# Performance work log

Measured on AMD Instinct MI355X. Metric: run time of the kernel, lower is better.

The kernel has to match this reference:

```python
import jax, jax.numpy as jnp
import numpy as np

E = 8      # num_experts
K = 2      # top-k
DIM = 1024
DFF = 2048  # fused gate+up width; intermediate = DFF // 2 == DIM


def setup_inputs() -> dict:
    key = jax.random.key(0)
    ks = jax.random.split(key, 5)
    B, S = 4, 2048
    x = jax.random.normal(ks[0], (B, S, DIM), dtype=jnp.float32)
    Wg = jax.random.normal(ks[1], (E, DIM), dtype=jnp.float32) * 0.02
    bg = jax.random.normal(ks[2], (E,), dtype=jnp.float32) * 0.02
    w1 = jax.random.normal(ks[3], (E, DFF, DIM), dtype=jnp.float32) * 0.02
    w2 = jax.random.normal(ks[4], (E, DIM, DFF // 2), dtype=jnp.float32) * 0.02
    return {"x": x, "Wg": Wg, "bg": bg, "w1": w1, "w2": w2}


def _moe(x, Wg, bg, w1, w2):
    B, S, D = x.shape
    t = x.reshape(-1, D)                      # [T, D] tokens
    logits = t @ Wg.T + bg                    # [T, E]
    probs = jax.nn.softmax(logits, axis=-1)
    topw, topi = jax.lax.top_k(probs, K)      # [T, K]
    topw = topw / jnp.sum(topw, axis=-1, keepdims=True)  # renormalize=True
    # per-token combine weight for each expert (0 if not selected): [T, E]
    combine = jnp.sum(jax.nn.one_hot(topi, E, dtype=t.dtype) * topw[..., None], axis=1)

    def body(acc, packed):
        w1e, w2e, ce = packed                 # [DFF, D], [D, DFF//2], [T]
        h = t @ w1e.T                         # [T, DFF]
        gate, up = jnp.split(h, 2, axis=-1)   # silu_and_mul (SwiGLU)
        a = jax.nn.silu(gate) * up            # [T, DFF//2]
        o = a @ w2e.T                         # [T, D]
        return acc + ce[:, None] * o, None

    out, _ = jax.lax.scan(body, jnp.zeros_like(t), (w1, w2, combine.T))
    return out.reshape(B, S, D)


def reference(x, Wg, bg, w1, w2):
    return _moe(x, Wg, bg, w1, w2)
```

## Files before the change

### kernel.cpp

```cpp
#include <hip/hip_runtime.h>
#include <hip/hip_bf16.h>
#include <cstdint>

#define T_TOKENS 8192
#define DIM 1024
#define NEXP 8
#define DFFH 1024
#define ROWCAP 17408
#define NCHUNK 16
#define MAXMT 24
#define NGATEB 128
#define NCASTB 1920

typedef __attribute__((ext_vector_type(8))) short bf16x8;
typedef __attribute__((ext_vector_type(16))) float f32x16;

__device__ __forceinline__ ushort f2bf(float f) {
  uint32_t u = __float_as_uint(f);
  uint32_t r = (u + 0x7fffu + ((u >> 16) & 1u)) >> 16;
  return (ushort)r;
}
__device__ __forceinline__ float bf2f(ushort u) {
  return __uint_as_float(((uint32_t)u) << 16);
}

__device__ __forceinline__ void async16(const void* g, const void* l) {
  __builtin_amdgcn_global_load_lds(
      (const __attribute__((address_space(1))) void*)(uintptr_t)g,
      (__attribute__((address_space(3))) void*)(uintptr_t)l, 16, 0, 0);
}

__global__ __launch_bounds__(256) void gatecast_kernel(
    const float4* __restrict__ x4, const float4* __restrict__ Wg4,
    const float* __restrict__ bg, const float4* __restrict__ w1,
    const float4* __restrict__ w2, int* __restrict__ top2e,
    float2* __restrict__ top2w, ushort* __restrict__ xb,
    ushort* __restrict__ w1b, ushort* __restrict__ w2b,
    int* __restrict__ blkcnt ) {
  __shared__ float4 wgl[NEXP * 256];
  __shared__ int lcnt[NEXP];
  const int tid = threadIdx.x;

  if (blockIdx.x >= NGATEB) {
    const int NW1 = NEXP * 2048 * DIM / 4;
    const int NW2 = NEXP * DIM * DFFH / 4;
    const int total = NW1 + NW2;
    const int cb = blockIdx.x - NGATEB;
    for (int i = cb * 256 + tid; i < total; i += NCASTB * 256) {
      float4 v; ushort* dst;
      if (i < NW1) { v = w1[i]; dst = w1b + (size_t)i * 4; }
      else { int j = i - NW1; v = w2[j]; dst = w2b + (size_t)j * 4; }
      ushort4 o4;
      o4.x = f2bf(v.x); o4.y = f2bf(v.y); o4.z = f2bf(v.z); o4.w = f2bf(v.w);
      *(ushort4*)dst = o4;
    }
    return;
  }

  for (int i = tid; i < NEXP * 256; i += 256) wgl[i] = Wg4[i];
  if (tid < NEXP) lcnt[tid] = 0;
  __syncthreads();
  const int wave = tid >> 6, lane = tid & 63;
  const float bgsel = bg[lane & 7];
  const int t0 = (blockIdx.x * 4 + wave) * 16;
  for (int tt = 0; tt < 16; ++tt) {
    const int t = t0 + tt;
    const float4* xr = x4 + (size_t)t * 256;
    ushort4* xw = (ushort4*)(xb + (size_t)t * DIM);
    float acc[NEXP];
#pragma unroll
    for (int e = 0; e < NEXP; ++e) acc[e] = 0.f;
#pragma unroll
    for (int j = 0; j < 4; ++j) {
      float4 xv = xr[lane + j * 64];
      ushort4 o4;
      o4.x = f2bf(xv.x); o4.y = f2bf(xv.y); o4.z = f2bf(xv.z); o4.w = f2bf(xv.w);
      xw[lane + j * 64] = o4;
#pragma unroll
      for (int e = 0; e < NEXP; ++e) {
        float4 wv = wgl[e * 256 + lane + j * 64];
        acc[e] += xv.x * wv.x + xv.y * wv.y + xv.z * wv.z + xv.w * wv.w;
      }
    }
#pragma unroll
    for (int e = 0; e < NEXP; ++e) {
      float v = acc[e];
      v += __shfl_xor(v, 1); v += __shfl_xor(v, 2); v += __shfl_xor(v, 4);
      acc[e] = v;
    }
    float v = acc[0];
#pragma unroll
    for (int e = 1; e < NEXP; ++e) v = ((lane & 7) == e) ? acc[e] : v;
    v += __shfl_xor(v, 8); v += __shfl_xor(v, 16); v += __shfl_xor(v, 32);
    v += bgsel;
    float m1 = v;
    m1 = fmaxf(m1, __shfl_xor(m1, 1));
    m1 = fmaxf(m1, __shfl_xor(m1, 2));
    m1 = fmaxf(m1, __shfl_xor(m1, 4));
    unsigned long long mk = __ballot(v == m1);
    int bi = (int)(__ffsll(mk) - 1) & 7;
    float v2 = (((lane & 7) == bi) ? -1e30f : v);
    float m2 = v2;
    m2 = fmaxf(m2, __shfl_xor(m2, 1));
    m2 = fmaxf(m2, __shfl_xor(m2, 2));
    m2 = fmaxf(m2, __shfl_xor(m2, 4));
    mk = __ballot(v2 == m2);
    int si = (int)(__ffsll(mk) - 1) & 7;
    if (lane == 0) {
      float w0 = 1.f / (1.f + __expf(m2 - m1));
      top2e[t] = bi | (si << 8);
      top2w[t] = make_float2(w0, 1.f - w0);
      atomicAdd(&lcnt[bi], 1);
      atomicAdd(&lcnt[si], 1);
    }
  }
  __syncthreads();
  if (tid < NEXP) blkcnt[blockIdx.x * NEXP + tid] = lcnt[tid];
}

__global__ __launch_bounds__(512) void scatter_kernel(
    const int* __restrict__ top2e, const float2* __restrict__ top2w,
    const int* __restrict__ blkcnt, int* __restrict__ rows_token,
    float* __restrict__ rows_weight, int2* __restrict__ tok2row,
    int* __restrict__ cnt, int* __restrict__ off) {
  __shared__ int s_all[NGATEB * NEXP];
  __shared__ int s_tot[NEXP], s_pre[NEXP];
  __shared__ int s_base[NEXP];
  __shared__ int lcnt[NEXP];
  const int tid = threadIdx.x;
  const int b = blockIdx.x;
  s_all[tid] = blkcnt[tid];
  s_all[512 + tid] = blkcnt[512 + tid];
  if (tid < NEXP) lcnt[tid] = 0;
  __syncthreads();
  if (tid < NEXP) {
    int tot = 0, pre = 0;
    const int cutoff = b * (NGATEB / NCHUNK);
#pragma unroll 1
    for (int k = 0; k < NGATEB; ++k) {
      int v = s_all[k * NEXP + tid];
      tot += v;
      if (k < cutoff) pre += v;
    }
    s_tot[tid] = tot; s_pre[tid] = pre;
  }
  __syncthreads();
  if (tid == 0) {
    int o = 0;
#pragma unroll
    for (int e = 0; e < NEXP; ++e) {
      s_base[e] = o + s_pre[e];
      if (b == 0) { cnt[e] = s_tot[e]; off[e] = o; }
      o += (s_tot[e] + 127) & ~127;
    }
    if (b == 0) off[NEXP] = o;
  }
  __syncthreads();
  const int t = b * 512 + tid;
  int pk = top2e[t];
  float2 w = top2w[t];
  int e0 = pk & 255, e1 = (pk >> 8) & 255;
  int p0 = atomicAdd(&lcnt[e0], 1);
  int p1 = atomicAdd(&lcnt[e1], 1);
  int r0 = s_base[e0] + p0;
  int r1 = s_base[e1] + p1;
  rows_token[r0] = t; rows_weight[r0] = w.x;
  rows_token[r1] = t; rows_weight[r1] = w.y;
  tok2row[t] = make_int2(r0, r1);
}

__global__ __launch_bounds__(256) void mlpA_kernel(
    const ushort* __restrict__ xb, const ushort* __restrict__ w1b,
    const int* __restrict__ rows_token, const int* __restrict__ cnt,
    const int* __restrict__ off, ushort* __restrict__ abuf) {
  const int bid = blockIdx.x;
  const int e = bid & 7;
  const int pos = bid >> 3;
  const int mt = pos >> 4, nt = pos & 15;
  const int count = cnt[e];
  if (mt * 128 >= count) return;
  const int base = off[e];

  __shared__ ushort As[2][128 * 64];
  __shared__ ushort Bs[2][2][64 * 64];

  const int tid = threadIdx.x;
  const int wave = tid >> 6, lane = tid & 63;
  const int wm = wave >> 1, wn = wave & 1;
  const int cg = tid & 7;
  const int r7w = (tid >> 3) & 7;
  const int cgs = (cg ^ r7w) * 8;

  const ushort* gA[4];
#pragma unroll
  for (int i = 0; i < 4; ++i) {
    int row = i * 32 + (tid >> 3);
    int r = mt * 128 + row;
    int tok = (r < count) ? rows_token[base + r] : 0;
    gA[i] = xb + ((size_t)tok * DIM + cgs);
  }
  const ushort* gBg[2];
  const ushort* gBu[2];
#pragma unroll
  for (int i = 0; i < 2; ++i) {
    int row = i * 32 + (tid >> 3);
    gBg[i] = w1b + ((size_t)(e * 2048 + nt * 64 + row) * DIM + cgs);
    gBu[i] = w1b + ((size_t)(e * 2048 + 1024 + nt * 64 + row) * DIM + cgs);
  }

#define STAGE_A1(b_, k0_)                                             \
  {                                                                   \
    _Pragma("unroll")                                                 \
    for (int i = 0; i < 4; ++i)                                       \
      async16(gA[i] + (k0_), &As[b_][(i * 256 + wave * 64) * 8]);     \
    _Pragma("unroll")                                                 \
    for (int i = 0; i < 2; ++i) {                                     \
      async16(gBg[i] + (k0_), &Bs[b_][0][(i * 256 + wave * 64) * 8]); \
      async16(gBu[i] + (k0_), &Bs[b_][1][(i * 256 + wave * 64) * 8]); \
    }                                                                 \
  }

  f32x16 accg0 = {0,0,0,0,0,0,0,0,0,0,0,0,0,0,0,0};
  f32x16 accg1 = accg0, accu0 = accg0, accu1 = accg0;

  const int xr = (lane & 7) << 3;
  const int la31 = lane & 31;
  const int kbase = (lane >> 5) * 8;

#define COMPA(b_)                                                              \
  {                                                                            \
    _Pragma("unroll")                                                          \
    for (int kk = 0; kk < 4; ++kk) {                                           \
      const int ko = (kk * 16 + kbase) ^ xr;                                   \
      bf16x8 a0 = *(const bf16x8*)&As[b_][(wm * 64 + la31) * 64 + ko];         \
      bf16x8 a1 = *(const bf16x8*)&As[b_][(wm * 64 + 32 + la31) * 64 + ko];    \
      bf16x8 bg_ = *(const bf16x8*)&Bs[b_][0][(wn * 32 + la31) * 64 + ko];     \
      bf16x8 bu_ = *(const bf16x8*)&Bs[b_][1][(wn * 32 + la31) * 64 + ko];     \
      accg0 = __builtin_amdgcn_mfma_f32_32x32x16_bf16(a0, bg_, accg0, 0, 0, 0);\
      accg1 = __builtin_amdgcn_mfma_f32_32x32x16_bf16(a1, bg_, accg1, 0, 0, 0);\
      accu0 = __builtin_amdgcn_mfma_f32_32x32x16_bf16(a0, bu_, accu0, 0, 0, 0);\
      accu1 = __builtin_amdgcn_mfma_f32_32x32x16_bf16(a1, bu_, accu1, 0, 0, 0);\
    }                                                                          \
  }

  STAGE_A1(0, 0);
  __syncthreads();
#pragma unroll
  for (int it = 0; it < 8; ++it) {
    STAGE_A1(1, it * 128 + 64);
    COMPA(0);
    __syncthreads();
    if (it < 7) STAGE_A1(0, it * 128 + 128);
    COMPA(1);
    __syncthreads();
  }

  const int colg = nt * 64 + wn * 32 + la31;
  const size_t rbase = (size_t)(base + mt * 128 + wm * 64);
  const int rlo = 4 * (lane >> 5);
#pragma unroll
  for (int s = 0; s < 2; ++s) {
    const f32x16 g16 = s ? accg1 : accg0;
    const f32x16 u16 = s ? accu1 : accu0;
#pragma unroll
    for (int r = 0; r < 16; ++r) {
      int rr = (r & 3) + 8 * (r >> 2) + rlo;
      float g = g16[r], u = u16[r];
      float a = (g / (1.f + __expf(-g))) * u;
      abuf[(rbase + s * 32 + rr) * DFFH + colg] = f2bf(a);
    }
  }
#undef STAGE_A1
#undef COMPA
}

__global__ __launch_bounds__(256) void mlpB_kernel(
    const ushort* __restrict__ abuf, const ushort* __restrict__ w2b,
    const float* __restrict__ rows_weight, const int* __restrict__ cnt,
    const int* __restrict__ off, ushort* __restrict__ obuf) {
  const int bid = blockIdx.x;
  const int e = bid & 7;
  const int pos = bid >> 3;
  const int mt = pos >> 3, nt = pos & 7;
  const int count = cnt[e];
  if (mt * 128 >= count) return;
  const int base = off[e];

  __shared__ ushort As[2][128 * 64];
  __shared__ ushort Bs[2][128 * 64];

  const int tid = threadIdx.x;
  const int wave = tid >> 6, lane = tid & 63;
  const int wm = wave >> 1, wn = wave & 1;
  const int cg = tid & 7;
  const int r7w = (tid >> 3) & 7;
  const int cgs = (cg ^ r7w) * 8;

  const ushort* gA[4];
#pragma unroll
  for (int i = 0; i < 4; ++i) {
    int row = i * 32 + (tid >> 3);
    gA[i] = abuf + ((size_t)(base + mt * 128 + row) * DFFH + cgs);
  }
  const ushort* gB[4];
#pragma unroll
  for (int i = 0; i < 4; ++i) {
    int row = i * 32 + (tid >> 3);
    gB[i] = w2b + ((size_t)(e * 1024 + nt * 128 + row) * DFFH + cgs);
  }

#define STAGE_B1(b_, k0_)                                           \
  {                                                                 \
    _Pragma("unroll")                                               \
    for (int i = 0; i < 4; ++i) {                                   \
      async16(gA[i] + (k0_), &As[b_][(i * 256 + wave * 64) * 8]);   \
      async16(gB[i] + (k0_), &Bs[b_][(i * 256 + wave * 64) * 8]);   \
    }                                                               \
  }

  f32x16 acc00 = {0,0,0,0,0,0,0,0,0,0,0,0,0,0,0,0};
  f32x16 acc01 = acc00, acc10 = acc00, acc11 = acc00;

  const int xr = (lane & 7) << 3;
  const int la31 = lane & 31;
  const int kbase = (lane >> 5) * 8;

#define COMPB(b_)                                                              \
  {                                                                            \
    _Pragma("unroll")                                                          \
    for (int kk = 0; kk < 4; ++kk) {                                           \
      const int ko = (kk * 16 + kbase) ^ xr;                                   \
      bf16x8 a0 = *(const bf16x8*)&As[b_][(wm * 64 + la31) * 64 + ko];         \
      bf16x8 a1 = *(const bf16x8*)&As[b_][(wm * 64 + 32 + la31) * 64 + ko];    \
      bf16x8 b0 = *(const bf16x8*)&Bs[b_][(wn * 64 + la31) * 64 + ko];         \
      bf16x8 b1 = *(const bf16x8*)&Bs[b_][(wn * 64 + 32 + la31) * 64 + ko];    \
      acc00 = __builtin_amdgcn_mfma_f32_32x32x16_bf16(a0, b0, acc00, 0, 0, 0); \
      acc01 = __builtin_amdgcn_mfma_f32_32x32x16_bf16(a0, b1, acc01, 0, 0, 0); \
      acc10 = __builtin_amdgcn_mfma_f32_32x32x16_bf16(a1, b0, acc10, 0, 0, 0); \
      acc11 = __builtin_amdgcn_mfma_f32_32x32x16_bf16(a1, b1, acc11, 0, 0, 0); \
    }                                                                          \
  }

  STAGE_B1(0, 0);
  __syncthreads();
#pragma unroll
  for (int it = 0; it < 8; ++it) {
    STAGE_B1(1, it * 128 + 64);
    COMPB(0);
    __syncthreads();
    if (it < 7) STAGE_B1(0, it * 128 + 128);
    COMPB(1);
    __syncthreads();
  }

  const int rlo = 4 * (lane >> 5);
  const int colb = nt * 128 + wn * 64 + la31;
#pragma unroll
  for (int s = 0; s < 2; ++s) {
    const f32x16 c0 = s ? acc10 : acc00;
    const f32x16 c1 = s ? acc11 : acc01;
#pragma unroll
    for (int r = 0; r < 16; ++r) {
      int rr = (r & 3) + 8 * (r >> 2) + rlo;
      int lrow = mt * 128 + wm * 64 + s * 32 + rr;
      if (lrow < count) {
        float wgt = rows_weight[base + lrow];
        obuf[(size_t)(base + lrow) * DIM + colb] = f2bf(wgt * c0[r]);
        obuf[(size_t)(base + lrow) * DIM + colb + 32] = f2bf(wgt * c1[r]);
      }
    }
  }
#undef STAGE_B1
#undef COMPB
}

__global__ __launch_bounds__(256) void combine_kernel(
    const ushort* __restrict__ obuf, const int2* __restrict__ tok2row,
    float* __restrict__ out) {
  const int t = blockIdx.x;
  int2 rr = tok2row[t];
  const ushort4* p0 = (const ushort4*)(obuf + (size_t)rr.x * DIM);
  const ushort4* p1 = (const ushort4*)(obuf + (size_t)rr.y * DIM);
  float4* po = (float4*)(out + (size_t)t * DIM);
  const int c = threadIdx.x;
  ushort4 a = p0[c], b = p1[c];
  float4 o;
  o.x = bf2f(a.x) + bf2f(b.x);
  o.y = bf2f(a.y) + bf2f(b.y);
  o.z = bf2f(a.z) + bf2f(b.z);
  o.w = bf2f(a.w) + bf2f(b.w);
  po[c] = o;
}

extern "C" void kernel_launch(void* const* d_in, const int* in_sizes, int n_in,
                              void* d_out, int out_size, void* d_ws, size_t ws_size,
                              hipStream_t stream) {
  const float* x = (const float*)d_in[0];
  const float* Wg = (const float*)d_in[1];
  const float* bg = (const float*)d_in[2];
  const float* w1 = (const float*)d_in[3];
  const float* w2 = (const float*)d_in[4];
  float* out = (float*)d_out;

  char* ws = (char*)d_ws;
  ushort* xb = (ushort*)ws;
  ushort* w1b = xb + (size_t)T_TOKENS * DIM;
  ushort* w2b = w1b + (size_t)NEXP * 2048 * DIM;
  ushort* abuf = w2b + (size_t)NEXP * DIM * DFFH;
  char* p = (char*)(abuf + (size_t)ROWCAP * DFFH);
  int* top2e = (int*)p;            p += T_TOKENS * 4;
  float2* top2w = (float2*)p;      p += T_TOKENS * 8;
  int* rows_token = (int*)p;       p += ROWCAP * 4;
  float* rows_weight = (float*)p;  p += ROWCAP * 4;
  int2* tok2row = (int2*)p;        p += T_TOKENS * 8;
  int* cnt = (int*)p;              p += 32;
  int* off = (int*)p;              p += 64;
  int* blkcnt = (int*)p;           p += NGATEB * NEXP * 4;
  ushort* obuf = xb;

  gatecast_kernel<<<NGATEB + NCASTB, 256, 0, stream>>>(
      (const float4*)x, (const float4*)Wg, bg, (const float4*)w1,
      (const float4*)w2, top2e, top2w, xb, w1b, w2b, blkcnt);
  scatter_kernel<<<NCHUNK, 512, 0, stream>>>(top2e, top2w, blkcnt, rows_token,
                                             rows_weight, tok2row, cnt, off);
  mlpA_kernel<<<8 * MAXMT * 16, 256, 0, stream>>>(xb, w1b, rows_token, cnt, off, abuf);
  mlpB_kernel<<<8 * MAXMT * 8, 256, 0, stream>>>(abuf, w2b, rows_weight, cnt, off, obuf);
  combine_kernel<<<T_TOKENS, 256, 0, stream>>>(obuf, tok2row, out);
}
```

Measured before the change: 231.6 us.

## Enlarge mlpA tile to 256x128 with 512-thread blocks

The first expert GEMM (gate/up plus SwiGLU) now uses 256-row by 128-column tiles per block with 8 waves, each wave computing a 128x32 slice for both gate and up. This raises arithmetic intensity per LDS load and halves the grid, cutting redundant global and LDS traffic for the weight and token tiles. Stores are masked to the padded per-expert row count because tiles can now overrun the 128-aligned padding. The cost is more LDS per block (about 128 KB) and more accumulator registers, which lowers occupancy and increases tail waste on partially filled expert tiles.

```diff
diff --git a/kernel.cpp b/kernel.cpp
--- a/kernel.cpp
+++ b/kernel.cpp
@@ -8,7 +8,8 @@
 #define DFFH 1024
 #define ROWCAP 17408
 #define NCHUNK 16
-#define MAXMT 24
+#define MAXMTA 12
+#define MAXMTB 24
 #define NGATEB 128
 #define NCASTB 1920
 
@@ -169,78 +170,87 @@
   tok2row[t] = make_int2(r0, r1);
 }
 
-__global__ __launch_bounds__(256) void mlpA_kernel(
+__global__ __launch_bounds__(512, 2) void mlpA_kernel(
     const ushort* __restrict__ xb, const ushort* __restrict__ w1b,
     const int* __restrict__ rows_token, const int* __restrict__ cnt,
     const int* __restrict__ off, ushort* __restrict__ abuf) {
   const int bid = blockIdx.x;
   const int e = bid & 7;
   const int pos = bid >> 3;
-  const int mt = pos >> 4, nt = pos & 15;
+  const int mt = pos >> 3, nt = pos & 7;
   const int count = cnt[e];
-  if (mt * 128 >= count) return;
+  if (mt * 256 >= count) return;
   const int base = off[e];
-
-  __shared__ ushort As[2][128 * 64];
-  __shared__ ushort Bs[2][2][64 * 64];
+  const int padcnt = off[e + 1] - base;
+
+  __shared__ ushort As[2][256 * 64];
+  __shared__ ushort Bg[2][128 * 64];
+  __shared__ ushort Bu[2][128 * 64];
 
   const int tid = threadIdx.x;
   const int wave = tid >> 6, lane = tid & 63;
-  const int wm = wave >> 1, wn = wave & 1;
+  const int wm = wave >> 2, wn = wave & 3;
   const int cg = tid & 7;
-  const int r7w = (tid >> 3) & 7;
-  const int cgs = (cg ^ r7w) * 8;
+  const int r7 = (tid >> 3) & 7;
+  const int cgs = (cg ^ r7) * 8;
 
   const ushort* gA[4];
 #pragma unroll
   for (int i = 0; i < 4; ++i) {
-    int row = i * 32 + (tid >> 3);
-    int r = mt * 128 + row;
+    int row = i * 64 + (tid >> 3);
+    int r = mt * 256 + row;
     int tok = (r < count) ? rows_token[base + r] : 0;
     gA[i] = xb + ((size_t)tok * DIM + cgs);
   }
-  const ushort* gBg[2];
-  const ushort* gBu[2];
+  const ushort* gG[2];
+  const ushort* gU[2];
 #pragma unroll
   for (int i = 0; i < 2; ++i) {
-    int row = i * 32 + (tid >> 3);
-    gBg[i] = w1b + ((size_t)(e * 2048 + nt * 64 + row) * DIM + cgs);
-    gBu[i] = w1b + ((size_t)(e * 2048 + 1024 + nt * 64 + row) * DIM + cgs);
-  }
-
-#define STAGE_A1(b_, k0_)                                             \
-  {                                                                   \
-    _Pragma("unroll")                                                 \
-    for (int i = 0; i < 4; ++i)                                       \
-      async16(gA[i] + (k0_), &As[b_][(i * 256 + wave * 64) * 8]);     \
-    _Pragma("unroll")                                                 \
-    for (int i = 0; i < 2; ++i) {                                     \
-      async16(gBg[i] + (k0_), &Bs[b_][0][(i * 256 + wave * 64) * 8]); \
-      async16(gBu[i] + (k0_), &Bs[b_][1][(i * 256 + wave * 64) * 8]); \
-    }                                                                 \
-  }
-
-  f32x16 accg0 = {0,0,0,0,0,0,0,0,0,0,0,0,0,0,0,0};
-  f32x16 accg1 = accg0, accu0 = accg0, accu1 = accg0;
+    int row = i * 64 + (tid >> 3);
+    gG[i] = w1b + ((size_t)(e * 2048 + nt * 128 + row) * DIM + cgs);
+    gU[i] = w1b + ((size_t)(e * 2048 + 1024 + nt * 128 + row) * DIM + cgs);
+  }
+
+#define STAGE_A1(b_, k0_)                                           \
+  {                                                                 \
+    _Pragma("unroll")                                               \
+    for (int i = 0; i < 4; ++i)                                     \
+      async16(gA[i] + (k0_), &As[b_][(i * 512 + tid) * 8]);         \
+    _Pragma("unroll")                                               \
+    for (int i = 0; i < 2; ++i) {                                   \
+      async16(gG[i] + (k0_), &Bg[b_][(i * 512 + tid) * 8]);         \
+      async16(gU[i] + (k0_), &Bu[b_][(i * 512 + tid) * 8]);         \
+    }                                                               \
+  }
+
+  const f32x16 zz = {0,0,0,0,0,0,0,0,0,0,0,0,0,0,0,0};
+  f32x16 ag[4] = {zz, zz, zz, zz};
+  f32x16 au[4] = {zz, zz, zz, zz};
 
   const int xr = (lane & 7) << 3;
   const int la31 = lane & 31;
   const int kbase = (lane >> 5) * 8;
 
-#define COMPA(b_)                                                              \
-  {                                                                            \
-    _Pragma("unroll")                                                          \
-    for (int kk = 0; kk < 4; ++kk) {                                           \
-      const int ko = (kk * 16 + kbase) ^ xr;                                   \
-      bf16x8 a0 = *(const bf16x8*)&As[b_][(wm * 64 + la31) * 64 + ko];         \
-      bf16x8 a1 = *(const bf16x8*)&As[b_][(wm * 64 + 32 + la31) * 64 + ko];    \
-      bf16x8 bg_ = *(const bf16x8*)&Bs[b_][0][(wn * 32 + la31) * 64 + ko];     \
-      bf16x8 bu_ = *(const bf16x8*)&Bs[b_][1][(wn * 32 + la31) * 64 + ko];     \
-      accg0 = __builtin_amdgcn_mfma_f32_32x32x16_bf16(a0, bg_, accg0, 0, 0, 0);\
-      accg1 = __builtin_amdgcn_mfma_f32_32x32x16_bf16(a1, bg_, accg1, 0, 0, 0);\
-      accu0 = __builtin_amdgcn_mfma_f32_32x32x16_bf16(a0, bu_, accu0, 0, 0, 0);\
-      accu1 = __builtin_amdgcn_mfma_f32_32x32x16_bf16(a1, bu_, accu1, 0, 0, 0);\
-    }                                                                          \
+#define COMPA(b_)                                                               \
+  {                                                                             \
+    _Pragma("unroll")                                                           \
+    for (int kk = 0; kk < 4; ++kk) {                                            \
+      const int ko = (kk * 16 + kbase) ^ xr;                                    \
+      bf16x8 bg_ = *(const bf16x8*)&Bg[b_][(wn * 32 + la31) * 64 + ko];         \
+      bf16x8 bu_ = *(const bf16x8*)&Bu[b_][(wn * 32 + la31) * 64 + ko];         \
+      bf16x8 a0 = *(const bf16x8*)&As[b_][(wm * 128 + la31) * 64 + ko];         \
+      bf16x8 a1 = *(const bf16x8*)&As[b_][(wm * 128 + 32 + la31) * 64 + ko];    \
+      bf16x8 a2 = *(const bf16x8*)&As[b_][(wm * 128 + 64 + la31) * 64 + ko];    \
+      bf16x8 a3 = *(const bf16x8*)&As[b_][(wm * 128 + 96 + la31) * 64 + ko];    \
+      ag[0] = __builtin_amdgcn_mfma_f32_32x32x16_bf16(a0, bg_, ag[0], 0, 0, 0); \
+      ag[1] = __builtin_amdgcn_mfma_f32_32x32x16_bf16(a1, bg_, ag[1], 0, 0, 0); \
+      ag[2] = __builtin_amdgcn_mfma_f32_32x32x16_bf16(a2, bg_, ag[2], 0, 0, 0); \
+      ag[3] = __builtin_amdgcn_mfma_f32_32x32x16_bf16(a3, bg_, ag[3], 0, 0, 0); \
+      au[0] = __builtin_amdgcn_mfma_f32_32x32x16_bf16(a0, bu_, au[0], 0, 0, 0); \
+      au[1] = __builtin_amdgcn_mfma_f32_32x32x16_bf16(a1, bu_, au[1], 0, 0, 0); \
+      au[2] = __builtin_amdgcn_mfma_f32_32x32x16_bf16(a2, bu_, au[2], 0, 0, 0); \
+      au[3] = __builtin_amdgcn_mfma_f32_32x32x16_bf16(a3, bu_, au[3], 0, 0, 0); \
+    }                                                                           \
   }
 
   STAGE_A1(0, 0);
@@ -255,19 +265,19 @@
     __syncthreads();
   }
 
-  const int colg = nt * 64 + wn * 32 + la31;
-  const size_t rbase = (size_t)(base + mt * 128 + wm * 64);
+  const int colg = nt * 128 + wn * 32 + la31;
   const int rlo = 4 * (lane >> 5);
 #pragma unroll
-  for (int s = 0; s < 2; ++s) {
-    const f32x16 g16 = s ? accg1 : accg0;
-    const f32x16 u16 = s ? accu1 : accu0;
+  for (int m = 0; m < 4; ++m) {
 #pragma unroll
     for (int r = 0; r < 16; ++r) {
       int rr = (r & 3) + 8 * (r >> 2) + rlo;
-      float g = g16[r], u = u16[r];
-      float a = (g / (1.f + __expf(-g))) * u;
-      abuf[(rbase + s * 32 + rr) * DFFH + colg] = f2bf(a);
+      int row = mt * 256 + wm * 128 + m * 32 + rr;
+      if (row < padcnt) {
+        float g = ag[m][r], u = au[m][r];
+        float a = (g / (1.f + __expf(-g))) * u;
+        abuf[(size_t)(base + row) * DFFH + colg] = f2bf(a);
+      }
     }
   }
 #undef STAGE_A1
@@ -423,7 +433,7 @@
       (const float4*)w2, top2e, top2w, xb, w1b, w2b, blkcnt);
   scatter_kernel<<<NCHUNK, 512, 0, stream>>>(top2e, top2w, blkcnt, rows_token,
                                              rows_weight, tok2row, cnt, off);
-  mlpA_kernel<<<8 * MAXMT * 16, 256, 0, stream>>>(xb, w1b, rows_token, cnt, off, abuf);
-  mlpB_kernel<<<8 * MAXMT * 8, 256, 0, stream>>>(abuf, w2b, rows_weight, cnt, off, obuf);
+  mlpA_kernel<<<8 * MAXMTA * 8, 512, 0, stream>>>(xb, w1b, rows_token, cnt, off, abuf);
+  mlpB_kernel<<<8 * MAXMTB * 8, 256, 0, stream>>>(abuf, w2b, rows_weight, cnt, off, obuf);
   combine_kernel<<<T_TOKENS, 256, 0, stream>>>(obuf, tok2row, out);
 }
```

After: 251.3 us. 8.5% more time.
